# Kernel optimization log

Hardware: AMD Instinct MI355X
Metric: run time of the kernel (lower is better)

## Reference

```python
import jax, jax.numpy as jnp
import numpy as np

HID = 128      # hidden_dim
CDIM = 128     # c_dim
NBLK = 5       # n_blocks
RESO = 32      # grid_resolution
G = RESO ** 3  # number of voxels
B, T = 2, 100000


def setup_inputs() -> dict:
    key = jax.random.key(0)
    ks = jax.random.split(key, 8)
    return {
        "points": jax.random.normal(ks[0], (B, T, 3), jnp.float32),
        "index": jax.random.randint(ks[1], (B, 1, T), 0, G, dtype=jnp.int64),
        # fc_pos: Linear(3, 2*HID)
        "fc_pos_w": jax.random.normal(ks[2], (3, 2 * HID), jnp.float32) * 0.1,
        "fc_pos_b": jnp.zeros((2 * HID,), jnp.float32),
        # ResnetBlockFC(2*HID, HID) x NBLK: fc_0 (2H->H), fc_1 (H->H), shortcut (2H->H, no bias)
        "fc0_w": jax.random.normal(ks[3], (NBLK, 2 * HID, HID), jnp.float32) * 0.05,
        "fc0_b": jnp.zeros((NBLK, HID), jnp.float32),
        "fc1_w": jax.random.normal(ks[4], (NBLK, HID, HID), jnp.float32) * 0.05,
        "fc1_b": jnp.zeros((NBLK, HID), jnp.float32),
        "sc_w": jax.random.normal(ks[5], (NBLK, 2 * HID, HID), jnp.float32) * 0.05,
        # fc_c: Linear(HID, CDIM)
        "fc_c_w": jax.random.normal(ks[6], (HID, CDIM), jnp.float32) * 0.05,
        "fc_c_b": jnp.zeros((CDIM,), jnp.float32),
    }


def _resnet_block(x, w0, b0, w1, b1, ws):
    # ResnetBlockFC: net = fc_0(relu(x)); dx = fc_1(relu(net)); out = shortcut(x) + dx
    net = jnp.maximum(x, 0.0) @ w0 + b0
    dx = jnp.maximum(net, 0.0) @ w1 + b1
    return x @ ws + dx


def reference(points, index, fc_pos_w, fc_pos_b, fc0_w, fc0_b, fc1_w, fc1_b, sc_w, fc_c_w, fc_c_b):
    idx = index[:, 0, :]  # [B, T]

    def pool_local(net):
        # scatter_max over voxels, then gather back per point
        seg = jax.vmap(lambda c_b, i_b: jax.ops.segment_max(c_b, i_b, num_segments=G))(net, idx)  # [B,G,H]
        return jnp.take_along_axis(seg, idx[:, :, None], axis=1)  # [B,T,H]; every gathered voxel is non-empty

    net = points @ fc_pos_w + fc_pos_b          # [B,T,2H]
    net = _resnet_block(net, fc0_w[0], fc0_b[0], fc1_w[0], fc1_b[0], sc_w[0])  # [B,T,H]
    for i in range(1, NBLK):
        pooled = pool_local(net)
        net = jnp.concatenate([net, pooled], axis=2)  # [B,T,2H]
        net = _resnet_block(net, fc0_w[i], fc0_b[i], fc1_w[i], fc1_b[i], sc_w[i])

    c = net @ fc_c_w + fc_c_b  # [B,T,CDIM]

    # generate_grid_features: scatter_mean into the 32^3 grid (zeros for empty voxels)
    sums = jax.vmap(lambda c_b, i_b: jax.ops.segment_sum(c_b, i_b, num_segments=G))(c, idx)  # [B,G,CDIM]
    cnts = jax.vmap(lambda i_b: jax.ops.segment_sum(jnp.ones((T,), c.dtype), i_b, num_segments=G))(idx)  # [B,G]
    cnts = cnts[:, :, None]
    mean = jnp.where(cnts > 0, sums / jnp.maximum(cnts, 1.0), 0.0)
    fea_grid = jnp.transpose(mean, (0, 2, 1)).reshape(B, CDIM, RESO, RESO, RESO)
    return fea_grid
```

## Files before the change

### kernel.cpp

```cpp
#include <hip/hip_runtime.h>

#define T_PTS 100000
#define NB 2
#define GCELLS 32768
#define NCELL (NB * GCELLS)
#define HID 128
#define MBLK 64
#define RBPB 1563
#define GRID_RB (NB * RBPB)

typedef __attribute__((ext_vector_type(8))) short bf16x8;
typedef __attribute__((ext_vector_type(4))) float f32x4;

#define MFMA16 __builtin_amdgcn_mfma_f32_16x16x32_bf16

__device__ __forceinline__ unsigned short bf16rne(float f) {
  unsigned u = __float_as_uint(f);
  return (unsigned short)((u + 0x7FFFu + ((u >> 16) & 1u)) >> 16);
}
__device__ __forceinline__ unsigned packhl(float f) {
  unsigned short h = bf16rne(f);
  float hf = __uint_as_float(((unsigned)h) << 16);
  unsigned short l = bf16rne(f - hf);
  return (((unsigned)h) << 16) | (unsigned)l;
}

union U8 { bf16x8 v; unsigned u[4]; };

template <int MODE>
__global__ __launch_bounds__(256, 3) void resblock_mfma(
    const void* __restrict__ srcv, const float* __restrict__ posw,
    const float* __restrict__ posb, const unsigned* __restrict__ cell,
    const int* __restrict__ idx, const unsigned short* __restrict__ w0p,
    const float* __restrict__ b0, const unsigned short* __restrict__ w1p,
    const float* __restrict__ b1, const unsigned short* __restrict__ swp,
    unsigned* __restrict__ net_out) {
  __shared__ unsigned short lds[16384];
  const int tid = threadIdx.x;
  const int lane = tid & 63;
  const int wc = tid >> 6;
  const int b = blockIdx.x / RBPB;
  const int t0 = (blockIdx.x % RBPB) * MBLK;
  const int valid = (T_PTS - t0 < MBLK) ? (T_PTS - t0) : MBLK;

  const int pt = tid >> 2;
  const int kc = (tid & 3) << 3;
  const int lstore = ((tid & 3) * 16 + (pt & 15)) ^ (tid & 3);
  const int sbase0 = (pt >> 4) * 512 + lstore * 8;
  const bool pv = (pt < valid);

  const unsigned* nrow = nullptr;
  const unsigned* crow = nullptr;
  float pp0 = 0.f, pp1 = 0.f, pp2 = 0.f;
  if (MODE == 1) {
    if (pv) {
      const long prow = (long)b * T_PTS + t0 + pt;
      nrow = (const unsigned*)srcv + prow * HID;
      crow = cell + ((long)b * GCELLS + idx[prow]) * HID;
    }
  } else {
    if (pv) {
      const float* ppp = (const float*)srcv + ((long)b * T_PTS + t0 + pt) * 3;
      pp0 = ppp[0]; pp1 = ppp[1]; pp2 = ppp[2];
    }
  }

  auto load_x = [&](int ks, unsigned* w) {
    if (MODE == 1) {
      if (pv) {
        const unsigned* rp = (ks < 4) ? (nrow + ks * 32 + kc)
                                      : (crow + (ks - 4) * 32 + kc);
        uint4 a = *(const uint4*)rp;
        uint4 c = *(const uint4*)(rp + 4);
        w[0] = a.x; w[1] = a.y; w[2] = a.z; w[3] = a.w;
        w[4] = c.x; w[5] = c.y; w[6] = c.z; w[7] = c.w;
      } else {
#pragma unroll
        for (int i = 0; i < 8; ++i) w[i] = 0u;
      }
    } else {
      const int kb = ks * 32 + kc;
      float xv[8];
#pragma unroll
      for (int i = 0; i < 8; i += 4) {
        float4 wa = *(const float4*)(posw + kb + i);
        float4 wb = *(const float4*)(posw + 256 + kb + i);
        float4 wcc = *(const float4*)(posw + 512 + kb + i);
        float4 bb = *(const float4*)(posb + kb + i);
        xv[i + 0] = fmaf(pp0, wa.x, fmaf(pp1, wb.x, fmaf(pp2, wcc.x, bb.x)));
        xv[i + 1] = fmaf(pp0, wa.y, fmaf(pp1, wb.y, fmaf(pp2, wcc.y, bb.y)));
        xv[i + 2] = fmaf(pp0, wa.z, fmaf(pp1, wb.z, fmaf(pp2, wcc.z, bb.z)));
        xv[i + 3] = fmaf(pp0, wa.w, fmaf(pp1, wb.w, fmaf(pp2, wcc.w, bb.w)));
      }
#pragma unroll
      for (int i = 0; i < 8; ++i) w[i] = pv ? packhl(xv[i]) : 0u;
    }
  };

  auto store_x = [&](int ks, const unsigned* w) {
    const int base = ((ks & 1) << 13) + sbase0;
    U8 vh, vl, vrh, vrl;
#pragma unroll
    for (int p = 0; p < 4; ++p) {
      const unsigned w0 = w[2 * p], w1 = w[2 * p + 1];
      const unsigned r0 = ((int)w0 < 0) ? 0u : w0;
      const unsigned r1 = ((int)w1 < 0) ? 0u : w1;
      vh.u[p] = __builtin_amdgcn_perm(w1, w0, 0x07060302u);
      vl.u[p] = __builtin_amdgcn_perm(w1, w0, 0x05040100u);
      vrh.u[p] = __builtin_amdgcn_perm(r1, r0, 0x07060302u);
      vrl.u[p] = __builtin_amdgcn_perm(r1, r0, 0x05040100u);
    }
    *(bf16x8*)(lds + base) = vh.v;
    *(bf16x8*)(lds + base + 2048) = vl.v;
    *(bf16x8*)(lds + base + 4096) = vrh.v;
    *(bf16x8*)(lds + base + 6144) = vrl.v;
  };

  auto load_B = [&](const unsigned short* base, int loOff, int ks, bf16x8* h,
                    bf16x8* l) {
#pragma unroll
    for (int nt = 0; nt < 2; ++nt) {
      const int fi = (ks * 8 + wc * 2 + nt) * 512 + lane * 8;
      h[nt] = *(const bf16x8*)(base + fi);
      l[nt] = *(const bf16x8*)(base + loOff + fi);
    }
  };

  f32x4 accy[4][2], acco[4][2];
#pragma unroll
  for (int i = 0; i < 4; ++i)
#pragma unroll
    for (int j = 0; j < 2; ++j) {
      f32x4 z = {0.f, 0.f, 0.f, 0.f};
      accy[i][j] = z;
      acco[i][j] = z;
    }

  {
    unsigned w[8];
    load_x(0, w);
    store_x(0, w);
  }
  __syncthreads();

  const int lar = lane ^ ((lane >> 4) & 3);
#pragma unroll 1
  for (int ks = 0; ks < 8; ++ks) {
    bf16x8 b1h[2], b1l[2], b2h[2], b2l[2];
    load_B(w0p, 32768, ks, b1h, b1l);
    load_B(swp, 32768, ks, b2h, b2l);
    unsigned nxt[8];
    if (ks < 7) load_x(ks + 1, nxt);
    const int sb = (ks & 1) << 13;
    __builtin_amdgcn_s_setprio(1);
#pragma unroll
    for (int mt = 0; mt < 4; ++mt) {
      const int ab = sb + mt * 512 + lar * 8;
      bf16x8 arh = *(const bf16x8*)(lds + ab + 4096);
      bf16x8 arl = *(const bf16x8*)(lds + ab + 6144);
#pragma unroll
      for (int nt = 0; nt < 2; ++nt) {
        accy[mt][nt] = MFMA16(arh, b1h[nt], accy[mt][nt], 0, 0, 0);
        accy[mt][nt] = MFMA16(arh, b1l[nt], accy[mt][nt], 0, 0, 0);
        accy[mt][nt] = MFMA16(arl, b1h[nt], accy[mt][nt], 0, 0, 0);
      }
    }
    __builtin_amdgcn_s_setprio(0);
    __builtin_amdgcn_s_setprio(1);
#pragma unroll
    for (int mt = 0; mt < 4; ++mt) {
      const int ab = sb + mt * 512 + lar * 8;
      bf16x8 axh = *(const bf16x8*)(lds + ab);
      bf16x8 axl = *(const bf16x8*)(lds + ab + 2048);
#pragma unroll
      for (int nt = 0; nt < 2; ++nt) {
        acco[mt][nt] = MFMA16(axh, b2h[nt], acco[mt][nt], 0, 0, 0);
        acco[mt][nt] = MFMA16(axh, b2l[nt], acco[mt][nt], 0, 0, 0);
        acco[mt][nt] = MFMA16(axl, b2h[nt], acco[mt][nt], 0, 0, 0);
      }
    }
    __builtin_amdgcn_s_setprio(0);
    if (ks < 7) store_x(ks + 1, nxt);
    __syncthreads();
  }

  {
    float b0v[2];
#pragma unroll
    for (int nt = 0; nt < 2; ++nt)
      b0v[nt] = b0[wc * 32 + nt * 16 + (lane & 15)];
#pragma unroll
    for (int mt = 0; mt < 4; ++mt) {
#pragma unroll
      for (int nt = 0; nt < 2; ++nt) {
        const int c = wc * 32 + nt * 16 + (lane & 15);
        const int k2 = c >> 5;
        const int j = c & 7;
        const int lahi = ((c & 31) >> 3) * 16;
#pragma unroll
        for (int r = 0; r < 4; ++r) {
          float h = fmaxf(accy[mt][nt][r] + b0v[nt], 0.f);
          unsigned short hh = bf16rne(h);
          float hf = __uint_as_float(((unsigned)hh) << 16);
          unsigned short hl = bf16rne(h - hf);
          int la = lahi + (lane >> 4) * 4 + r;
          la ^= (la >> 3) & 7;
          const int o = ((k2 * 4 + mt) * 64 + la) * 8 + j;
          lds[o] = hh;
          lds[o + 8192] = hl;
        }
      }
    }
  }
  __syncthreads();

  {
    const int lar2 = lane ^ ((lane >> 3) & 7);
#pragma unroll
    for (int k2 = 0; k2 < 4; ++k2) {
      bf16x8 ch[2], cl[2];
      load_B(w1p, 16384, k2, ch, cl);
      __builtin_amdgcn_s_setprio(1);
#pragma unroll
      for (int mt = 0; mt < 4; ++mt) {
        const int ab = ((k2 * 4 + mt) * 64 + lar2) * 8;
        bf16x8 ah = *(const bf16x8*)(lds + ab);
        bf16x8 al = *(const bf16x8*)(lds + ab + 8192);
#pragma unroll
        for (int nt = 0; nt < 2; ++nt) {
          acco[mt][nt] = MFMA16(ah, ch[nt], acco[mt][nt], 0, 0, 0);
          acco[mt][nt] = MFMA16(ah, cl[nt], acco[mt][nt], 0, 0, 0);
          acco[mt][nt] = MFMA16(al, ch[nt], acco[mt][nt], 0, 0, 0);
        }
      }
      __builtin_amdgcn_s_setprio(0);
    }
  }

  {
    float b1v[2];
#pragma unroll
    for (int nt = 0; nt < 2; ++nt)
      b1v[nt] = b1[wc * 32 + nt * 16 + (lane & 15)];
#pragma unroll
    for (int mt = 0; mt < 4; ++mt) {
#pragma unroll
      for (int r = 0; r < 4; ++r) {
        const int row = mt * 16 + (lane >> 4) * 4 + r;
        if (row < valid) {
          unsigned* op = net_out + ((long)b * T_PTS + t0 + row) * HID;
          op[wc * 32 + (lane & 15)] = packhl(acco[mt][0][r] + b1v[0]);
          op[wc * 32 + 16 + (lane & 15)] = packhl(acco[mt][1][r] + b1v[1]);
        }
      }
    }
  }
}

__global__ __launch_bounds__(256, 4) void final_mfma(
    unsigned* __restrict__ net, const unsigned short* __restrict__ wcp,
    const float* __restrict__ bc) {
  __shared__ unsigned short lds[8192];
  const int tid = threadIdx.x;
  const int lane = tid & 63;
  const int wc = tid >> 6;
  const int b = blockIdx.x / RBPB;
  const int t0 = (blockIdx.x % RBPB) * MBLK;
  const int valid = (T_PTS - t0 < MBLK) ? (T_PTS - t0) : MBLK;

  const int pt = tid >> 2;
  const int kc = (tid & 3) << 3;
  const int lstore = ((tid & 3) * 16 + (pt & 15)) ^ (tid & 3);
  const int sbase0 = (pt >> 4) * 512 + lstore * 8;
  const bool pv = (pt < valid);
  const unsigned* nrow = pv ? net + ((long)b * T_PTS + t0 + pt) * HID : nullptr;

  auto load_x = [&](int ks, unsigned* w) {
    if (pv) {
      const unsigned* rp = nrow + ks * 32 + kc;
      uint4 a = *(const uint4*)rp;
      uint4 c = *(const uint4*)(rp + 4);
      w[0] = a.x; w[1] = a.y; w[2] = a.z; w[3] = a.w;
      w[4] = c.x; w[5] = c.y; w[6] = c.z; w[7] = c.w;
    } else {
#pragma unroll
      for (int i = 0; i < 8; ++i) w[i] = 0u;
    }
  };
  auto store_x = [&](int ks, const unsigned* w) {
    const int base = ((ks & 1) << 12) + sbase0;
    U8 vh, vl;
#pragma unroll
    for (int p = 0; p < 4; ++p) {
      const unsigned w0 = w[2 * p], w1 = w[2 * p + 1];
      vh.u[p] = __builtin_amdgcn_perm(w1, w0, 0x07060302u);
      vl.u[p] = __builtin_amdgcn_perm(w1, w0, 0x05040100u);
    }
    *(bf16x8*)(lds + base) = vh.v;
    *(bf16x8*)(lds + base + 2048) = vl.v;
  };
  auto load_B = [&](int ks, bf16x8* h, bf16x8* l) {
#pragma unroll
    for (int nt = 0; nt < 2; ++nt) {
      const int fi = (ks * 8 + wc * 2 + nt) * 512 + lane * 8;
      h[nt] = *(const bf16x8*)(wcp + fi);
      l[nt] = *(const bf16x8*)(wcp + 16384 + fi);
    }
  };

  f32x4 acc[4][2];
#pragma unroll
  for (int i = 0; i < 4; ++i)
#pragma unroll
    for (int j = 0; j < 2; ++j) {
      f32x4 z = {0.f, 0.f, 0.f, 0.f};
      acc[i][j] = z;
    }

  {
    unsigned w[8];
    load_x(0, w);
    store_x(0, w);
  }
  __syncthreads();

  const int lar = lane ^ ((lane >> 4) & 3);
#pragma unroll 1
  for (int ks = 0; ks < 4; ++ks) {
    bf16x8 ch[2], cl[2];
    load_B(ks, ch, cl);
    unsigned nxt[8];
    if (ks < 3) load_x(ks + 1, nxt);
    const int sb = (ks & 1) << 12;
    __builtin_amdgcn_s_setprio(1);
#pragma unroll
    for (int mt = 0; mt < 4; ++mt) {
      const int ab = sb + mt * 512 + lar * 8;
      bf16x8 ah = *(const bf16x8*)(lds + ab);
      bf16x8 al = *(const bf16x8*)(lds + ab + 2048);
#pragma unroll
      for (int nt = 0; nt < 2; ++nt) {
        acc[mt][nt] = MFMA16(ah, ch[nt], acc[mt][nt], 0, 0, 0);
        acc[mt][nt] = MFMA16(ah, cl[nt], acc[mt][nt], 0, 0, 0);
        acc[mt][nt] = MFMA16(al, ch[nt], acc[mt][nt], 0, 0, 0);
      }
    }
    __builtin_amdgcn_s_setprio(0);
    if (ks < 3) store_x(ks + 1, nxt);
    __syncthreads();
  }

  float* fout = (float*)net;
  float bcv[2];
#pragma unroll
  for (int nt = 0; nt < 2; ++nt)
    bcv[nt] = bc[wc * 32 + nt * 16 + (lane & 15)];
#pragma unroll
  for (int mt = 0; mt < 4; ++mt) {
#pragma unroll
    for (int r = 0; r < 4; ++r) {
      const int row = mt * 16 + (lane >> 4) * 4 + r;
      if (row < valid) {
        float* op = fout + ((long)b * T_PTS + t0 + row) * HID;
        op[wc * 32 + (lane & 15)] = acc[mt][0][r] + bcv[0];
        op[wc * 32 + 16 + (lane & 15)] = acc[mt][1][r] + bcv[1];
      }
    }
  }
}

__global__ void pack_weights(const float* __restrict__ fc0,
                             const float* __restrict__ fc1,
                             const float* __restrict__ sc,
                             const float* __restrict__ fcc,
                             unsigned short* __restrict__ w0p,
                             unsigned short* __restrict__ w1p,
                             unsigned short* __restrict__ swp,
                             unsigned short* __restrict__ wcp) {
  int gid = blockIdx.x * 256 + threadIdx.x;
  const float* src;
  unsigned short* dst;
  int K, e;
  if (gid < 163840) { src = fc0; dst = w0p; K = 256; e = gid; }
  else if (gid < 327680) { src = sc; dst = swp; K = 256; e = gid - 163840; }
  else if (gid < 409600) { src = fc1; dst = w1p; K = 128; e = gid - 327680; }
  else if (gid < 425984) { src = fcc; dst = wcp; K = 128; e = gid - 409600; }
  else return;
  const int mat = e / (K * 128);
  const int r = e - mat * K * 128;
  const int k = r >> 7, n = r & 127;
  const float x = src[e];
  const unsigned short hi = bf16rne(x);
  const float hf = __uint_as_float(((unsigned)hi) << 16);
  const unsigned short lo = bf16rne(x - hf);
  const int ks = k >> 5, lg = (k >> 3) & 3, j = k & 7;
  const int l = lg * 16 + (n & 15), nt = n >> 4;
  unsigned short* mb = dst + (long)mat * K * 256;
  const int off = ((ks * 8 + nt) * 64 + l) * 8 + j;
  mb[off] = hi;
  mb[off + K * 128] = lo;
}

__global__ void zero_i32(int* __restrict__ p, int n) {
  const int i = blockIdx.x * 256 + threadIdx.x;
  if (i < n) p[i] = 0;
}

__global__ void count_csr(const int* __restrict__ idx, int* __restrict__ curs) {
  const int gid = blockIdx.x * 256 + threadIdx.x;
  if (gid >= NB * T_PTS) return;
  const int b = gid / T_PTS;
  atomicAdd(&curs[b * GCELLS + idx[gid]], 1);
}

__global__ __launch_bounds__(1024) void scan_csr(const int* __restrict__ cnt,
                                                 int* __restrict__ offsets) {
  __shared__ int part[1024];
  const int t = threadIdx.x;
  const int base = t * (NCELL / 1024);
  int s = 0;
  for (int i = 0; i < NCELL / 1024; ++i) s += cnt[base + i];
  part[t] = s;
  __syncthreads();
  for (int d = 1; d < 1024; d <<= 1) {
    int v = (t >= d) ? part[t - d] : 0;
    __syncthreads();
    part[t] += v;
    __syncthreads();
  }
  int run = (t == 0) ? 0 : part[t - 1];
  for (int i = 0; i < NCELL / 1024; ++i) {
    offsets[base + i] = run;
    run += cnt[base + i];
  }
  if (t == 1023) offsets[NCELL] = run;
}

__global__ void scatter_csr(const int* __restrict__ idx,
                            const int* __restrict__ offsets,
                            int* __restrict__ curs, int* __restrict__ perm) {
  const int gid = blockIdx.x * 256 + threadIdx.x;
  if (gid >= NB * T_PTS) return;
  const int b = gid / T_PTS;
  const int cellk = b * GCELLS + idx[gid];
  const int slot = offsets[cellk] + atomicAdd(&curs[cellk], 1);
  perm[slot] = gid;
}

__global__ __launch_bounds__(256) void pool_csr(const unsigned* __restrict__ net,
                                                const int* __restrict__ perm,
                                                const int* __restrict__ offsets,
                                                unsigned* __restrict__ cellf) {
  const int cellk = blockIdx.x * 4 + (threadIdx.x >> 6);
  const int lane = threadIdx.x & 63;
  const int s0 = offsets[cellk], s1 = offsets[cellk + 1];
  if (s0 >= s1) return;
  float m0 = -3.402823466e38f, m1 = -3.402823466e38f;
  unsigned b0 = 0u, b1 = 0u;
  for (int j = s0; j < s1; ++j) {
    const long row = perm[j];
    uint2 w = *(const uint2*)(net + row * HID + lane * 2);
    float v0 = __uint_as_float(w.x & 0xFFFF0000u) + __uint_as_float(w.x << 16);
    float v1 = __uint_as_float(w.y & 0xFFFF0000u) + __uint_as_float(w.y << 16);
    if (v0 > m0) { m0 = v0; b0 = w.x; }
    if (v1 > m1) { m1 = v1; b1 = w.y; }
  }
  uint2 o; o.x = b0; o.y = b1;
  *(uint2*)(cellf + (long)cellk * HID + lane * 2) = o;
}

__global__ __launch_bounds__(256) void cellsum_csr(
    const float* __restrict__ c, const int* __restrict__ perm,
    const int* __restrict__ offsets, float* __restrict__ sums) {
  const int cellk = blockIdx.x * 4 + (threadIdx.x >> 6);
  const int lane = threadIdx.x & 63;
  const int s0 = offsets[cellk], s1 = offsets[cellk + 1];
  if (s0 >= s1) return;
  float2 m = {0.f, 0.f};
  for (int j = s0; j < s1; ++j) {
    const long row = perm[j];
    float2 v = *(const float2*)(c + row * HID + lane * 2);
    m.x += v.x;
    m.y += v.y;
  }
  *(float2*)(sums + (long)cellk * HID + lane * 2) = m;
}

__global__ void mean_kernel(const float* __restrict__ sums,
                            const int* __restrict__ offsets,
                            float* __restrict__ out) {
  const long gid = (long)blockIdx.x * 256 + threadIdx.x;
  if (gid >= (long)NB * HID * GCELLS) return;
  const int g = (int)(gid % GCELLS);
  const int c = (int)((gid / GCELLS) % HID);
  const int b = (int)(gid / ((long)HID * GCELLS));
  const int cellk = b * GCELLS + g;
  const int cnt = offsets[cellk + 1] - offsets[cellk];
  out[gid] = cnt > 0 ? sums[(long)cellk * HID + c] / (float)cnt : 0.f;
}

extern "C" void kernel_launch(void* const* d_in, const int* in_sizes, int n_in,
                              void* d_out, int out_size, void* d_ws,
                              size_t ws_size, hipStream_t stream) {
  const float* points = (const float*)d_in[0];
  const int* idx = (const int*)d_in[1];
  const float* fc_pos_w = (const float*)d_in[2];
  const float* fc_pos_b = (const float*)d_in[3];
  const float* fc0_w = (const float*)d_in[4];
  const float* fc0_b = (const float*)d_in[5];
  const float* fc1_w = (const float*)d_in[6];
  const float* fc1_b = (const float*)d_in[7];
  const float* sc_w = (const float*)d_in[8];
  const float* fc_c_w = (const float*)d_in[9];
  const float* fc_c_b = (const float*)d_in[10];
  float* out = (float*)d_out;

  const long NET_BYTES = (long)NB * T_PTS * HID * 4;
  const long CELL_BYTES = (long)NB * GCELLS * HID * 4;
  unsigned* net = (unsigned*)d_ws;
  unsigned* cellf = (unsigned*)((char*)d_ws + NET_BYTES);
  float* sums = (float*)cellf;
  int* offsets = (int*)((char*)d_ws + NET_BYTES + CELL_BYTES);

  unsigned short* packs = (unsigned short*)d_out;
  unsigned short* w0p = packs;
  unsigned short* swp = packs + 327680;
  unsigned short* w1p = packs + 655360;
  unsigned short* wcp = packs + 819200;
  int* curs = (int*)((char*)d_out + (2l << 20));
  int* perm = (int*)((char*)d_out + (3l << 20));

  const int GRID_PTS = (NB * T_PTS + 255) / 256;
  const int GRID_ZERO = (NCELL + 255) / 256;
  const int GRID_CELL = NCELL / 4;
  const int GRID_MEAN = NB * HID * GCELLS / 256;

  pack_weights<<<1664, 256, 0, stream>>>(fc0_w, fc1_w, sc_w, fc_c_w, w0p, w1p,
                                         swp, wcp);

  zero_i32<<<GRID_ZERO, 256, 0, stream>>>(curs, NCELL);
  count_csr<<<GRID_PTS, 256, 0, stream>>>(idx, curs);
  scan_csr<<<1, 1024, 0, stream>>>(curs, offsets);
  zero_i32<<<GRID_ZERO, 256, 0, stream>>>(curs, NCELL);
  scatter_csr<<<GRID_PTS, 256, 0, stream>>>(idx, offsets, curs, perm);

  resblock_mfma<0><<<GRID_RB, 256, 0, stream>>>(
      points, fc_pos_w, fc_pos_b, nullptr, nullptr, w0p, fc0_b, w1p, fc1_b,
      swp, net);

  for (int i = 1; i < 5; ++i) {
    pool_csr<<<GRID_CELL, 256, 0, stream>>>(net, perm, offsets, cellf);
    resblock_mfma<1><<<GRID_RB, 256, 0, stream>>>(
        net, nullptr, nullptr, cellf, idx, w0p + (long)i * 65536,
        fc0_b + i * HID, w1p + (long)i * 32768, fc1_b + i * HID,
        swp + (long)i * 65536, net);
  }

  final_mfma<<<GRID_RB, 256, 0, stream>>>(net, wcp, fc_c_b);
  cellsum_csr<<<GRID_CELL, 256, 0, stream>>>((const float*)net, perm, offsets,
                                             sums);
  mean_kernel<<<GRID_MEAN, 256, 0, stream>>>(sums, offsets, out);
}
```

Measured before the change: 776.4 us.

## Store packed hi/lo words in LDS and split to bf16 on read

The staged activations are now kept in LDS as packed 32-bit hi/lo words, written straight from the global loads, instead of as four pre-split bf16 planes (hi, lo, relu-hi, relu-lo). The hi/lo split and the relu are done with perm instructions after each LDS read, just before the MFMAs, and the two GEMM loops of the first matmul stage are merged so one LDS read feeds both. Out-of-range points now clamp to the last valid row instead of branching to zeros. This halves the LDS footprint and the store traffic, but adds VALU perm and select work inside the MFMA loop and changes the LDS access patterns, which may introduce bank conflicts.

```diff
diff --git a/kernel.cpp b/kernel.cpp
--- a/kernel.cpp
+++ b/kernel.cpp
@@ -27,6 +27,12 @@
 
 union U8 { bf16x8 v; unsigned u[4]; };
 
+__device__ __forceinline__ void up2(unsigned w0, unsigned w1, unsigned& h,
+                                    unsigned& l) {
+  h = __builtin_amdgcn_perm(w1, w0, 0x07060302u);
+  l = __builtin_amdgcn_perm(w1, w0, 0x05040100u);
+}
+
 template <int MODE>
 __global__ __launch_bounds__(256, 3) void resblock_mfma(
     const void* __restrict__ srcv, const float* __restrict__ posw,
@@ -35,49 +41,38 @@
     const float* __restrict__ b0, const unsigned short* __restrict__ w1p,
     const float* __restrict__ b1, const unsigned short* __restrict__ swp,
     unsigned* __restrict__ net_out) {
-  __shared__ unsigned short lds[16384];
+  __shared__ unsigned lds32[8192];
   const int tid = threadIdx.x;
   const int lane = tid & 63;
-  const int wc = tid >> 6;
+  const int wid = tid >> 6;
+  const int wc = wid;
   const int b = blockIdx.x / RBPB;
   const int t0 = (blockIdx.x % RBPB) * MBLK;
   const int valid = (T_PTS - t0 < MBLK) ? (T_PTS - t0) : MBLK;
 
   const int pt = tid >> 2;
   const int kc = (tid & 3) << 3;
-  const int lstore = ((tid & 3) * 16 + (pt & 15)) ^ (tid & 3);
-  const int sbase0 = (pt >> 4) * 512 + lstore * 8;
-  const bool pv = (pt < valid);
-
+  const int ptc = (t0 + pt < T_PTS) ? pt : (T_PTS - 1 - t0);
   const unsigned* nrow = nullptr;
   const unsigned* crow = nullptr;
   float pp0 = 0.f, pp1 = 0.f, pp2 = 0.f;
   if (MODE == 1) {
-    if (pv) {
-      const long prow = (long)b * T_PTS + t0 + pt;
-      nrow = (const unsigned*)srcv + prow * HID;
-      crow = cell + ((long)b * GCELLS + idx[prow]) * HID;
-    }
+    const long prow = (long)b * T_PTS + t0 + ptc;
+    nrow = (const unsigned*)srcv + prow * HID;
+    crow = cell + ((long)b * GCELLS + idx[prow]) * HID;
   } else {
-    if (pv) {
-      const float* ppp = (const float*)srcv + ((long)b * T_PTS + t0 + pt) * 3;
-      pp0 = ppp[0]; pp1 = ppp[1]; pp2 = ppp[2];
-    }
+    const float* ppp = (const float*)srcv + ((long)b * T_PTS + t0 + ptc) * 3;
+    pp0 = ppp[0]; pp1 = ppp[1]; pp2 = ppp[2];
   }
 
   auto load_x = [&](int ks, unsigned* w) {
     if (MODE == 1) {
-      if (pv) {
-        const unsigned* rp = (ks < 4) ? (nrow + ks * 32 + kc)
-                                      : (crow + (ks - 4) * 32 + kc);
-        uint4 a = *(const uint4*)rp;
-        uint4 c = *(const uint4*)(rp + 4);
-        w[0] = a.x; w[1] = a.y; w[2] = a.z; w[3] = a.w;
-        w[4] = c.x; w[5] = c.y; w[6] = c.z; w[7] = c.w;
-      } else {
-#pragma unroll
-        for (int i = 0; i < 8; ++i) w[i] = 0u;
-      }
+      const unsigned* rp = (ks < 4) ? (nrow + ks * 32 + kc)
+                                    : (crow + (ks - 4) * 32 + kc);
+      uint4 a = *(const uint4*)rp;
+      uint4 c = *(const uint4*)(rp + 4);
+      w[0] = a.x; w[1] = a.y; w[2] = a.z; w[3] = a.w;
+      w[4] = c.x; w[5] = c.y; w[6] = c.z; w[7] = c.w;
     } else {
       const int kb = ks * 32 + kc;
       float xv[8];
@@ -93,27 +88,17 @@
         xv[i + 3] = fmaf(pp0, wa.w, fmaf(pp1, wb.w, fmaf(pp2, wcc.w, bb.w)));
       }
 #pragma unroll
-      for (int i = 0; i < 8; ++i) w[i] = pv ? packhl(xv[i]) : 0u;
+      for (int i = 0; i < 8; ++i) w[i] = packhl(xv[i]);
     }
   };
 
   auto store_x = [&](int ks, const unsigned* w) {
-    const int base = ((ks & 1) << 13) + sbase0;
-    U8 vh, vl, vrh, vrl;
-#pragma unroll
-    for (int p = 0; p < 4; ++p) {
-      const unsigned w0 = w[2 * p], w1 = w[2 * p + 1];
-      const unsigned r0 = ((int)w0 < 0) ? 0u : w0;
-      const unsigned r1 = ((int)w1 < 0) ? 0u : w1;
-      vh.u[p] = __builtin_amdgcn_perm(w1, w0, 0x07060302u);
-      vl.u[p] = __builtin_amdgcn_perm(w1, w0, 0x05040100u);
-      vrh.u[p] = __builtin_amdgcn_perm(r1, r0, 0x07060302u);
-      vrl.u[p] = __builtin_amdgcn_perm(r1, r0, 0x05040100u);
-    }
-    *(bf16x8*)(lds + base) = vh.v;
-    *(bf16x8*)(lds + base + 2048) = vl.v;
-    *(bf16x8*)(lds + base + 4096) = vrh.v;
-    *(bf16x8*)(lds + base + 6144) = vrl.v;
+    unsigned* p = &lds32[((ks & 1) << 11) + wid * 512 + lane * 4];
+    uint4 q;
+    q.x = w[0]; q.y = w[1]; q.z = w[2]; q.w = w[3];
+    *(uint4*)p = q;
+    q.x = w[4]; q.y = w[5]; q.z = w[6]; q.w = w[7];
+    *(uint4*)(p + 256) = q;
   };
 
   auto load_B = [&](const unsigned short* base, int loOff, int ks, bf16x8* h,
@@ -143,7 +128,7 @@
   }
   __syncthreads();
 
-  const int lar = lane ^ ((lane >> 4) & 3);
+  const int lam = (lane & 15) * 4 + (lane >> 4);
 #pragma unroll 1
   for (int ks = 0; ks < 8; ++ks) {
     bf16x8 b1h[2], b1l[2], b2h[2], b2l[2];
@@ -151,32 +136,34 @@
     load_B(swp, 32768, ks, b2h, b2l);
     unsigned nxt[8];
     if (ks < 7) load_x(ks + 1, nxt);
-    const int sb = (ks & 1) << 13;
+    const int sb = (ks & 1) << 11;
     __builtin_amdgcn_s_setprio(1);
 #pragma unroll
     for (int mt = 0; mt < 4; ++mt) {
-      const int ab = sb + mt * 512 + lar * 8;
-      bf16x8 arh = *(const bf16x8*)(lds + ab + 4096);
-      bf16x8 arl = *(const bf16x8*)(lds + ab + 6144);
+      const unsigned* p = &lds32[sb + mt * 512 + lam * 4];
+      uint4 q1 = *(const uint4*)p;
+      uint4 q2 = *(const uint4*)(p + 256);
+      unsigned q[8] = {q1.x, q1.y, q1.z, q1.w, q2.x, q2.y, q2.z, q2.w};
+      U8 xh, xl, rh, rl;
+#pragma unroll
+      for (int p2 = 0; p2 < 4; ++p2) {
+        const unsigned w0 = q[2 * p2], w1 = q[2 * p2 + 1];
+        const unsigned r0 = ((int)w0 < 0) ? 0u : w0;
+        const unsigned r1 = ((int)w1 < 0) ? 0u : w1;
+        up2(w0, w1, xh.u[p2], xl.u[p2]);
+        up2(r0, r1, rh.u[p2], rl.u[p2]);
+      }
 #pragma unroll
       for (int nt = 0; nt < 2; ++nt) {
-        accy[mt][nt] = MFMA16(arh, b1h[nt], accy[mt][nt], 0, 0, 0);
-        accy[mt][nt] = MFMA16(arh, b1l[nt], accy[mt][nt], 0, 0, 0);
-        accy[mt][nt] = MFMA16(arl, b1h[nt], accy[mt][nt], 0, 0, 0);
-      }
-    }
-    __builtin_amdgcn_s_setprio(0);
-    __builtin_amdgcn_s_setprio(1);
-#pragma unroll
-    for (int mt = 0; mt < 4; ++mt) {
-      const int ab = sb + mt * 512 + lar * 8;
-      bf16x8 axh = *(const bf16x8*)(lds + ab);
-      bf16x8 axl = *(const bf16x8*)(lds + ab + 2048);
+        accy[mt][nt] = MFMA16(rh.v, b1h[nt], accy[mt][nt], 0, 0, 0);
+        accy[mt][nt] = MFMA16(rh.v, b1l[nt], accy[mt][nt], 0, 0, 0);
+        accy[mt][nt] = MFMA16(rl.v, b1h[nt], accy[mt][nt], 0, 0, 0);
+      }
 #pragma unroll
       for (int nt = 0; nt < 2; ++nt) {
-        acco[mt][nt] = MFMA16(axh, b2h[nt], acco[mt][nt], 0, 0, 0);
-        acco[mt][nt] = MFMA16(axh, b2l[nt], acco[mt][nt], 0, 0, 0);
-        acco[mt][nt] = MFMA16(axl, b2h[nt], acco[mt][nt], 0, 0, 0);
+        acco[mt][nt] = MFMA16(xh.v, b2h[nt], acco[mt][nt], 0, 0, 0);
+        acco[mt][nt] = MFMA16(xh.v, b2l[nt], acco[mt][nt], 0, 0, 0);
+        acco[mt][nt] = MFMA16(xl.v, b2h[nt], acco[mt][nt], 0, 0, 0);
       }
     }
     __builtin_amdgcn_s_setprio(0);
@@ -200,14 +187,9 @@
 #pragma unroll
         for (int r = 0; r < 4; ++r) {
           float h = fmaxf(accy[mt][nt][r] + b0v[nt], 0.f);
-          unsigned short hh = bf16rne(h);
-          float hf = __uint_as_float(((unsigned)hh) << 16);
-          unsigned short hl = bf16rne(h - hf);
           int la = lahi + (lane >> 4) * 4 + r;
           la ^= (la >> 3) & 7;
-          const int o = ((k2 * 4 + mt) * 64 + la) * 8 + j;
-          lds[o] = hh;
-          lds[o + 8192] = hl;
+          lds32[((k2 * 4 + mt) * 64 + la) * 8 + j] = packhl(h);
         }
       }
     }
@@ -223,14 +205,19 @@
       __builtin_amdgcn_s_setprio(1);
 #pragma unroll
       for (int mt = 0; mt < 4; ++mt) {
-        const int ab = ((k2 * 4 + mt) * 64 + lar2) * 8;
-        bf16x8 ah = *(const bf16x8*)(lds + ab);
-        bf16x8 al = *(const bf16x8*)(lds + ab + 8192);
+        const unsigned* p = &lds32[((k2 * 4 + mt) * 64 + lar2) * 8];
+        uint4 q1 = *(const uint4*)p;
+        uint4 q2 = *(const uint4*)(p + 4);
+        unsigned q[8] = {q1.x, q1.y, q1.z, q1.w, q2.x, q2.y, q2.z, q2.w};
+        U8 ah, al;
+#pragma unroll
+        for (int p2 = 0; p2 < 4; ++p2)
+          up2(q[2 * p2], q[2 * p2 + 1], ah.u[p2], al.u[p2]);
 #pragma unroll
         for (int nt = 0; nt < 2; ++nt) {
-          acco[mt][nt] = MFMA16(ah, ch[nt], acco[mt][nt], 0, 0, 0);
-          acco[mt][nt] = MFMA16(ah, cl[nt], acco[mt][nt], 0, 0, 0);
-          acco[mt][nt] = MFMA16(al, ch[nt], acco[mt][nt], 0, 0, 0);
+          acco[mt][nt] = MFMA16(ah.v, ch[nt], acco[mt][nt], 0, 0, 0);
+          acco[mt][nt] = MFMA16(ah.v, cl[nt], acco[mt][nt], 0, 0, 0);
+          acco[mt][nt] = MFMA16(al.v, ch[nt], acco[mt][nt], 0, 0, 0);
         }
       }
       __builtin_amdgcn_s_setprio(0);
@@ -260,44 +247,34 @@
 __global__ __launch_bounds__(256, 4) void final_mfma(
     unsigned* __restrict__ net, const unsigned short* __restrict__ wcp,
     const float* __restrict__ bc) {
-  __shared__ unsigned short lds[8192];
+  __shared__ unsigned lds32[4096];
   const int tid = threadIdx.x;
   const int lane = tid & 63;
-  const int wc = tid >> 6;
+  const int wid = tid >> 6;
+  const int wc = wid;
   const int b = blockIdx.x / RBPB;
   const int t0 = (blockIdx.x % RBPB) * MBLK;
   const int valid = (T_PTS - t0 < MBLK) ? (T_PTS - t0) : MBLK;
 
   const int pt = tid >> 2;
   const int kc = (tid & 3) << 3;
-  const int lstore = ((tid & 3) * 16 + (pt & 15)) ^ (tid & 3);
-  const int sbase0 = (pt >> 4) * 512 + lstore * 8;
-  const bool pv = (pt < valid);
-  const unsigned* nrow = pv ? net + ((long)b * T_PTS + t0 + pt) * HID : nullptr;
+  const int ptc = (t0 + pt < T_PTS) ? pt : (T_PTS - 1 - t0);
+  const unsigned* nrow = net + ((long)b * T_PTS + t0 + ptc) * HID;
 
   auto load_x = [&](int ks, unsigned* w) {
-    if (pv) {
-      const unsigned* rp = nrow + ks * 32 + kc;
-      uint4 a = *(const uint4*)rp;
-      uint4 c = *(const uint4*)(rp + 4);
-      w[0] = a.x; w[1] = a.y; w[2] = a.z; w[3] = a.w;
-      w[4] = c.x; w[5] = c.y; w[6] = c.z; w[7] = c.w;
-    } else {
-#pragma unroll
-      for (int i = 0; i < 8; ++i) w[i] = 0u;
-    }
+    const unsigned* rp = nrow + ks * 32 + kc;
+    uint4 a = *(const uint4*)rp;
+    uint4 c = *(const uint4*)(rp + 4);
+    w[0] = a.x; w[1] = a.y; w[2] = a.z; w[3] = a.w;
+    w[4] = c.x; w[5] = c.y; w[6] = c.z; w[7] = c.w;
   };
   auto store_x = [&](int ks, const unsigned* w) {
-    const int base = ((ks & 1) << 12) + sbase0;
-    U8 vh, vl;
-#pragma unroll
-    for (int p = 0; p < 4; ++p) {
-      const unsigned w0 = w[2 * p], w1 = w[2 * p + 1];
-      vh.u[p] = __builtin_amdgcn_perm(w1, w0, 0x07060302u);
-      vl.u[p] = __builtin_amdgcn_perm(w1, w0, 0x05040100u);
-    }
-    *(bf16x8*)(lds + base) = vh.v;
-    *(bf16x8*)(lds + base + 2048) = vl.v;
+    unsigned* p = &lds32[((ks & 1) << 11) + wid * 512 + lane * 4];
+    uint4 q;
+    q.x = w[0]; q.y = w[1]; q.z = w[2]; q.w = w[3];
+    *(uint4*)p = q;
+    q.x = w[4]; q.y = w[5]; q.z = w[6]; q.w = w[7];
+    *(uint4*)(p + 256) = q;
   };
   auto load_B = [&](int ks, bf16x8* h, bf16x8* l) {
 #pragma unroll
@@ -324,25 +301,30 @@
   }
   __syncthreads();
 
-  const int lar = lane ^ ((lane >> 4) & 3);
+  const int lam = (lane & 15) * 4 + (lane >> 4);
 #pragma unroll 1
   for (int ks = 0; ks < 4; ++ks) {
     bf16x8 ch[2], cl[2];
     load_B(ks, ch, cl);
     unsigned nxt[8];
     if (ks < 3) load_x(ks + 1, nxt);
-    const int sb = (ks & 1) << 12;
+    const int sb = (ks & 1) << 11;
     __builtin_amdgcn_s_setprio(1);
 #pragma unroll
     for (int mt = 0; mt < 4; ++mt) {
-      const int ab = sb + mt * 512 + lar * 8;
-      bf16x8 ah = *(const bf16x8*)(lds + ab);
-      bf16x8 al = *(const bf16x8*)(lds + ab + 2048);
+      const unsigned* p = &lds32[sb + mt * 512 + lam * 4];
+      uint4 q1 = *(const uint4*)p;
+      uint4 q2 = *(const uint4*)(p + 256);
+      unsigned q[8] = {q1.x, q1.y, q1.z, q1.w, q2.x, q2.y, q2.z, q2.w};
+      U8 ah, al;
+#pragma unroll
+      for (int p2 = 0; p2 < 4; ++p2)
+        up2(q[2 * p2], q[2 * p2 + 1], ah.u[p2], al.u[p2]);
 #pragma unroll
       for (int nt = 0; nt < 2; ++nt) {
-        acc[mt][nt] = MFMA16(ah, ch[nt], acc[mt][nt], 0, 0, 0);
-        acc[mt][nt] = MFMA16(ah, cl[nt], acc[mt][nt], 0, 0, 0);
-        acc[mt][nt] = MFMA16(al, ch[nt], acc[mt][nt], 0, 0, 0);
+        acc[mt][nt] = MFMA16(ah.v, ch[nt], acc[mt][nt], 0, 0, 0);
+        acc[mt][nt] = MFMA16(ah.v, cl[nt], acc[mt][nt], 0, 0, 0);
+        acc[mt][nt] = MFMA16(al.v, ch[nt], acc[mt][nt], 0, 0, 0);
       }
     }
     __builtin_amdgcn_s_setprio(0);
```

Result: slower. 800.6 us (+3.1%).
